# Kernel optimization log

Measured on AMD Instinct MI355X. Metric: run time of the kernel, lower is better.

The kernel has to match this reference:

```python
import jax, jax.numpy as jnp
import numpy as np

# ---------- static mesh topology helpers (numpy, setup-time only) ----------

def _topo_subdivide(nv, faces):
    edge_id = {}
    mids = []
    nf = []
    def mid(a, b):
        k = (a, b) if a < b else (b, a)
        if k not in edge_id:
            edge_id[k] = nv + len(mids)
            mids.append(k)
        return edge_id[k]
    for a, b, c in faces:
        a, b, c = int(a), int(b), int(c)
        ab, bc, ca = mid(a, b), mid(b, c), mid(c, a)
        nf += [[a, ab, ca], [b, bc, ab], [c, ca, bc], [ab, bc, ca]]
    return np.array(nf, dtype=np.int64), np.array(mids, dtype=np.int64)

def _icosphere(level, radius):
    t = (1.0 + 5.0 ** 0.5) / 2.0
    v = np.array([[-1, t, 0], [1, t, 0], [-1, -t, 0], [1, -t, 0],
                  [0, -1, t], [0, 1, t], [0, -1, -t], [0, 1, -t],
                  [t, 0, -1], [t, 0, 1], [-t, 0, -1], [-t, 0, 1]], dtype=np.float64)
    v /= np.linalg.norm(v, axis=1, keepdims=True)
    f = np.array([[0, 11, 5], [0, 5, 1], [0, 1, 7], [0, 7, 10], [0, 10, 11],
                  [1, 5, 9], [5, 11, 4], [11, 10, 2], [10, 7, 6], [7, 1, 8],
                  [3, 9, 4], [3, 4, 2], [3, 2, 6], [3, 6, 8], [3, 8, 9],
                  [4, 9, 5], [2, 4, 11], [6, 2, 10], [8, 6, 7], [9, 8, 1]], dtype=np.int64)
    for _ in range(level):
        f, mids = _topo_subdivide(len(v), f)
        mv = v[mids[:, 0]] + v[mids[:, 1]]
        mv /= np.linalg.norm(mv, axis=1, keepdims=True)
        v = np.concatenate([v, mv], 0)
    return (v * radius).astype(np.float32), f

def _directed_edges(faces):
    e = np.concatenate([faces[:, [0, 1]], faces[:, [1, 2]], faces[:, [2, 0]],
                        faces[:, [1, 0]], faces[:, [2, 1]], faces[:, [0, 2]]], 0)
    return np.unique(e, axis=0).T.astype(np.int64)  # (2, E) directed, deduped

# ---------- jax forward math ----------

def _project(verts, camera_c, camera_f):
    # K @ [I | t], t = (0,0,0.8): rows [f0,0,c0,0.8*c0],[0,f1,c1,0.8*c1],[0,0,1,0.8]
    z = jnp.zeros((), verts.dtype); o = jnp.ones((), verts.dtype)
    tz = jnp.asarray(0.8, verts.dtype)
    P = jnp.stack([
        jnp.stack([camera_f[0], z, camera_c[0], tz * camera_c[0]]),
        jnp.stack([z, camera_f[1], camera_c[1], tz * camera_c[1]]),
        jnp.stack([z, z, o, tz])])
    hom = jnp.concatenate([verts, jnp.ones((verts.shape[0], 1), verts.dtype)], 1)
    pc = hom @ P.T                     # (V, 3)
    return pc[:, :2] / pc[:, 2:3]      # (V, 2) pixel coords [x, y]

def _bilerp(feat, px, py, image_size):
    # feat: (C, dim, dim); px, py: (V,)
    dim = feat.shape[1]
    x = px * dim / image_size
    y = py * dim / image_size
    x1 = jnp.floor(x); x2 = x1 + 1.0
    y1 = jnp.floor(y); y2 = y1 + 1.0
    xi1 = jnp.clip(x1.astype(jnp.int32), 0, dim - 1)
    xi2 = jnp.clip(x2.astype(jnp.int32), 0, dim - 1)
    yi1 = jnp.clip(y1.astype(jnp.int32), 0, dim - 1)
    yi2 = jnp.clip(y2.astype(jnp.int32), 0, dim - 1)
    f11 = feat[:, xi1, yi1].T  # (V, C)
    f12 = feat[:, xi1, yi2].T
    f21 = feat[:, xi2, yi1].T
    f22 = feat[:, xi2, yi2].T
    w11 = ((x2 - x) * (y2 - y))[:, None]
    w12 = ((x2 - x) * (y - y1))[:, None]
    w21 = ((x - x1) * (y2 - y))[:, None]
    w22 = ((x - x1) * (y - y1))[:, None]
    return w11 * f11 + w12 * f12 + w21 * f21 + w22 * f22

def _gconv(x, W0, W1, b, src, dst):
    agg = jax.ops.segment_sum(x[dst], src, num_segments=x.shape[0])
    return x @ W0 + agg @ W1 + b

def _gresnet(x, edges, params):
    Win0, Win1, bin_, W0s, W1s, bs, Wc0, Wc1, bc = params
    src, dst = edges[0], edges[1]
    h = jax.nn.relu(_gconv(x, Win0, Win1, bin_, src, dst))
    def body(h, lw):
        W0, W1, b = lw
        return jax.nn.relu(_gconv(h, W0, W1, b, src, dst)) + h, None
    h, _ = jax.lax.scan(body, h, (W0s, W1s, bs))
    coords = _gconv(h, Wc0, Wc1, bc, src, dst)
    return h, coords

def _forward(f3, f4, f5, verts0, camera_c, camera_f, p1, p2, p3,
             edges1, edges2, edges3, mid0, mid1, image_size):
    def deform(verts, shape_feat, edges, params):
        pix = _project(verts, camera_c, camera_f)
        px, py = pix[:, 0], pix[:, 1]
        perc = jnp.concatenate([_bilerp(f3, px, py, image_size),
                                _bilerp(f4, px, py, image_size),
                                _bilerp(f5, px, py, image_size)], 1)  # (V, 1280)
        feats = jnp.concatenate([perc, shape_feat], 1)
        h, coords = _gresnet(feats, edges, params)
        return coords, h
    def unpool(verts, feat, mid):
        vf = jnp.concatenate([verts, feat], 1)
        new = (vf[mid[:, 0]] + vf[mid[:, 1]]) * 0.5  # edge midpoints
        vf = jnp.concatenate([vf, new], 0)
        return vf[:, :3], vf[:, 3:]
    verts, feat = deform(verts0, verts0, edges1, p1)
    verts, feat = unpool(verts, feat, mid0)
    verts, feat = deform(verts, feat, edges2, p2)
    verts, feat = unpool(verts, feat, mid1)
    verts, _ = deform(verts, feat, edges3, p3)
    return verts  # (40962, 3)

# ---------- harness entry points ----------

def setup_inputs() -> dict:
    key = jax.random.key(0)
    keys = iter(jax.random.split(key, 64))
    v0, f0 = _icosphere(4, 0.2)                      # 2562 verts, 5120 faces
    f1, mid0 = _topo_subdivide(len(v0), f0)          # -> 10242 verts topology
    f2, mid1 = _topo_subdivide(len(v0) + len(mid0), f1)  # -> 40962 verts
    inp = {
        'f3': jax.random.normal(next(keys), (256, 56, 56), jnp.float32),
        'f4': jax.random.normal(next(keys), (512, 28, 28), jnp.float32),
        'f5': jax.random.normal(next(keys), (512, 14, 14), jnp.float32),
        'verts0': jnp.asarray(v0),
        'camera_c': jnp.array([112.0, 112.0], jnp.float32),
        'camera_f': jnp.array([248.0, 248.0], jnp.float32),
    }
    D, L = 128, 12
    def stage(prefix, in_dim):
        def w(shape, scale):
            return jax.random.normal(next(keys), shape, jnp.float32) * scale
        inp[prefix + '_Win0'] = w((in_dim, D), 1.0 / np.sqrt(in_dim))
        inp[prefix + '_Win1'] = w((in_dim, D), 1.0 / np.sqrt(in_dim))
        inp[prefix + '_bin'] = jnp.zeros((D,), jnp.float32)
        inp[prefix + '_W0'] = w((L, D, D), 0.3 / np.sqrt(D))
        inp[prefix + '_W1'] = w((L, D, D), 0.3 / np.sqrt(D))
        inp[prefix + '_b'] = jnp.zeros((L, D), jnp.float32)
        inp[prefix + '_Wc0'] = w((D, 3), 0.01 / np.sqrt(D))
        inp[prefix + '_Wc1'] = w((D, 3), 0.01 / np.sqrt(D))
        inp[prefix + '_bc'] = jnp.zeros((3,), jnp.float32)
    stage('g1', 1283)
    stage('g2', 1408)
    stage('g3', 1408)
    inp['edges1'] = jnp.asarray(_directed_edges(f0))   # (2, 15360)
    inp['edges2'] = jnp.asarray(_directed_edges(f1))   # (2, 61440)
    inp['edges3'] = jnp.asarray(_directed_edges(f2))   # (2, 245760)
    inp['mid0'] = jnp.asarray(mid0)                    # (7680, 2)
    inp['mid1'] = jnp.asarray(mid1)                    # (30720, 2)
    inp['image_size'] = 224
    return inp

def reference(f3, f4, f5, verts0, camera_c, camera_f,
              g1_Win0, g1_Win1, g1_bin, g1_W0, g1_W1, g1_b, g1_Wc0, g1_Wc1, g1_bc,
              g2_Win0, g2_Win1, g2_bin, g2_W0, g2_W1, g2_b, g2_Wc0, g2_Wc1, g2_bc,
              g3_Win0, g3_Win1, g3_bin, g3_W0, g3_W1, g3_b, g3_Wc0, g3_Wc1, g3_bc,
              edges1, edges2, edges3, mid0, mid1, image_size):
    p1 = (g1_Win0, g1_Win1, g1_bin, g1_W0, g1_W1, g1_b, g1_Wc0, g1_Wc1, g1_bc)
    p2 = (g2_Win0, g2_Win1, g2_bin, g2_W0, g2_W1, g2_b, g2_Wc0, g2_Wc1, g2_bc)
    p3 = (g3_Win0, g3_Win1, g3_bin, g3_W0, g3_W1, g3_b, g3_Wc0, g3_Wc1, g3_bc)
    return _forward(f3, f4, f5, verts0, camera_c, camera_f, p1, p2, p3,
                    edges1, edges2, edges3, mid0, mid1, image_size)
```

## Files before the change

kernel.cpp:

```cpp
#include <hip/hip_runtime.h>
#include <hip/hip_bf16.h>
#include <cstddef>
#include <cstdint>

#define DIV_UP(a, b) (((a) + (b) - 1) / (b))

typedef __attribute__((ext_vector_type(8))) short bf16x8v;
typedef __attribute__((ext_vector_type(4))) float f32x4v;

__device__ __forceinline__ unsigned short bf16_rn(float v) {
    unsigned int u = __float_as_uint(v);
    unsigned int r = (u + 0x7FFFu + ((u >> 16) & 1u)) >> 16;
    return (unsigned short)r;
}
__device__ __forceinline__ float bf16_f(unsigned short h) {
    return __uint_as_float(((unsigned int)h) << 16);
}
__device__ __forceinline__ void f2hl(float v, unsigned short& hi, unsigned short& lo) {
    hi = bf16_rn(v);
    float r = v - bf16_f(hi);
    lo = bf16_rn(r);
}
__device__ __forceinline__ int xcd_swz(int orig, int nwg) {
    int q = nwg >> 3, r = nwg & 7;
    int xcd = orig & 7, idx = orig >> 3;
    return (xcd < r ? xcd * (q + 1) : r * (q + 1) + (xcd - r) * q) + idx;
}

__global__ void transpose_hl(const float* __restrict__ in, unsigned short* __restrict__ ohi,
                             unsigned short* __restrict__ olo, int C, int HW) {
    int idx = blockIdx.x * 256 + threadIdx.x;
    if (idx >= C * HW) return;
    int c = idx % C;
    int p = idx / C;
    float v = in[(size_t)c * HW + p];
    unsigned short hi, lo;
    f2hl(v, hi, lo);
    ohi[(size_t)p * C + c] = hi;
    olo[(size_t)p * C + c] = lo;
}

struct PackArgs {
    const float* Win0[3]; const float* Win1[3];
    const float* W0L[3];  const float* W1L[3];
    unsigned short *BtLhi[3], *BtLlo[3];
    unsigned short *BtShi[2], *BtSlo[2];
    unsigned short *Bgh[3], *Bgl[3];
};

__global__ void pack_all(PackArgs p) {
    const int LAY1 = 12 * 128 * 256;
    const int LAYT = 3 * LAY1;
    const int SH1 = 256 * 128;
    const int SHT = 2 * SH1;
    const int GB0 = 768 * 256, GB1 = 768 * 512;
    int idx = blockIdx.x * 256 + threadIdx.x;
    float v;
    unsigned short* dh;
    unsigned short* dl;
    size_t o;
    if (idx < LAYT) {
        int st = idx / LAY1, r = idx % LAY1;
        int l = r >> 15, rr = r & 32767;
        int n = rr >> 8, k = rr & 255;
        v = (k < 128) ? p.W0L[st][(size_t)l * 16384 + k * 128 + n]
                      : p.W1L[st][(size_t)l * 16384 + (k - 128) * 128 + n];
        dh = p.BtLhi[st]; dl = p.BtLlo[st]; o = r;
    } else if (idx < LAYT + SHT) {
        int q = idx - LAYT;
        int st = q / SH1, rr = q % SH1;
        int n = rr >> 7, k = rr & 127;
        const float* w0 = p.Win0[st + 1];
        const float* w1 = p.Win1[st + 1];
        v = (n < 128) ? w0[(size_t)(1280 + k) * 128 + n]
                      : w1[(size_t)(1280 + k) * 128 + (n - 128)];
        dh = p.BtShi[st]; dl = p.BtSlo[st]; o = rr;
    } else {
        int q = idx - LAYT - SHT;
        int m, C, base;
        if (q < GB0) { m = 0; C = 256; base = 0; }
        else if (q < GB0 + GB1) { m = 1; C = 512; base = 256; q -= GB0; }
        else if (q < GB0 + 2 * GB1) { m = 2; C = 512; base = 768; q -= GB0 + GB1; }
        else return;
        int n = q / C, k = q % C;
        int s = n >> 8, j = n & 255;
        v = (j < 128) ? p.Win0[s][(size_t)(base + k) * 128 + j]
                      : p.Win1[s][(size_t)(base + k) * 128 + (j - 128)];
        dh = p.Bgh[m]; dl = p.Bgl[m]; o = q;
    }
    unsigned short hi, lo;
    f2hl(v, hi, lo);
    dh[o] = hi;
    dl[o] = lo;
}

__global__ void desc_adj_kernel(const float* __restrict__ verts,
                                const float* __restrict__ cam_c, const float* __restrict__ cam_f,
                                const int* __restrict__ imgsz, int V,
                                const int* __restrict__ src, const int* __restrict__ dst, int E,
                                int* __restrict__ sampi, float* __restrict__ sampw,
                                int* __restrict__ adj8) {
    int v = blockIdx.x * 256 + threadIdx.x;
    if (v >= V) return;
    float X = verts[3 * v + 0], Yy = verts[3 * v + 1], Z = verts[3 * v + 2];
    float cx = cam_c[0], cy = cam_c[1], fx = cam_f[0], fy = cam_f[1];
    const float tz = 0.8f;
    float pz = Z + tz;
    float px = (fx * X + cx * Z + tz * cx) / pz;
    float py = (fy * Yy + cy * Z + tz * cy) / pz;
    float is = (float)imgsz[0];
    const int Ss[3] = {56, 28, 14};
#pragma unroll
    for (int m = 0; m < 3; ++m) {
        int S = Ss[m];
        float dim = (float)S;
        float x = px * dim / is;
        float y = py * dim / is;
        float x1 = floorf(x), y1 = floorf(y);
        float x2 = x1 + 1.0f, y2 = y1 + 1.0f;
        float smax = (float)(S - 1);
        int xi1 = (int)fminf(fmaxf(x1, 0.0f), smax);
        int xi2 = (int)fminf(fmaxf(x2, 0.0f), smax);
        int yi1 = (int)fminf(fmaxf(y1, 0.0f), smax);
        int yi2 = (int)fminf(fmaxf(y2, 0.0f), smax);
        int b = v * 12 + m * 4;
        sampi[b + 0] = xi1 * S + yi1;
        sampi[b + 1] = xi1 * S + yi2;
        sampi[b + 2] = xi2 * S + yi1;
        sampi[b + 3] = xi2 * S + yi2;
        sampw[b + 0] = (x2 - x) * (y2 - y);
        sampw[b + 1] = (x2 - x) * (y - y1);
        sampw[b + 2] = (x - x1) * (y2 - y);
        sampw[b + 3] = (x - x1) * (y - y1);
    }
    int lo = 0, hi = E;
    while (lo < hi) { int m = (lo + hi) >> 1; if (src[m] < v) lo = m + 1; else hi = m; }
    int e0 = lo;
    hi = E;
    while (lo < hi) { int m = (lo + hi) >> 1; if (src[m] < v + 1) lo = m + 1; else hi = m; }
    int e1 = lo;
    int* ap = adj8 + (size_t)v * 8;
#pragma unroll
    for (int i = 0; i < 8; ++i) {
        int e = e0 + i;
        ap[i] = (e < e1) ? dst[e] : -1;
    }
}

struct MArgs {
    const unsigned short *Ahi, *Alo; int lda;
    const unsigned short *Bhi, *Blo; int K;
    float* Y;
    int sstr;
    int V;
};

template <int EPI>
__global__ __launch_bounds__(256) void mgemm(MArgs g) {
    __shared__ unsigned short As_hi[64][40], As_lo[64][40];
    __shared__ unsigned short Bs_hi[128][40], Bs_lo[128][40];
    int tid = threadIdx.x;
    int row0 = blockIdx.y * 64;
    int col0 = blockIdx.x * 128;
    int l = tid & 63, wid = tid >> 6;
    int wr = wid & 1, wc = wid >> 1;
    int lw = l & 15, gg = l >> 4;
    f32x4v acc[2][4];
#pragma unroll
    for (int i = 0; i < 2; ++i)
#pragma unroll
        for (int j = 0; j < 4; ++j) acc[i][j] = (f32x4v){0.f, 0.f, 0.f, 0.f};

    int arow = tid >> 2, akoff = (tid & 3) * 8;
    for (int k0 = 0; k0 < g.K; k0 += 32) {
        __syncthreads();
        {
            int grow = row0 + arow;
            uint4 zh = make_uint4(0, 0, 0, 0), zl = make_uint4(0, 0, 0, 0);
            if (grow < g.V) {
                zh = *(const uint4*)(g.Ahi + (size_t)grow * g.lda + k0 + akoff);
                zl = *(const uint4*)(g.Alo + (size_t)grow * g.lda + k0 + akoff);
            }
            *(uint4*)&As_hi[arow][akoff] = zh;
            *(uint4*)&As_lo[arow][akoff] = zl;
        }
#pragma unroll
        for (int it = 0; it < 2; ++it) {
            int q = tid + it * 256;
            int n = q >> 2, koff = (q & 3) * 8;
            *(uint4*)&Bs_hi[n][koff] = *(const uint4*)(g.Bhi + (size_t)(col0 + n) * g.K + k0 + koff);
            *(uint4*)&Bs_lo[n][koff] = *(const uint4*)(g.Blo + (size_t)(col0 + n) * g.K + k0 + koff);
        }
        __syncthreads();
        bf16x8v ah[2], al[2], bh[4], bl[4];
#pragma unroll
        for (int mt = 0; mt < 2; ++mt) {
            int r = wr * 32 + mt * 16 + lw;
            ah[mt] = *(const bf16x8v*)&As_hi[r][gg * 8];
            al[mt] = *(const bf16x8v*)&As_lo[r][gg * 8];
        }
#pragma unroll
        for (int nt = 0; nt < 4; ++nt) {
            int c = wc * 64 + nt * 16 + lw;
            bh[nt] = *(const bf16x8v*)&Bs_hi[c][gg * 8];
            bl[nt] = *(const bf16x8v*)&Bs_lo[c][gg * 8];
        }
#pragma unroll
        for (int mt = 0; mt < 2; ++mt)
#pragma unroll
            for (int nt = 0; nt < 4; ++nt) {
                acc[mt][nt] = __builtin_amdgcn_mfma_f32_16x16x32_bf16(ah[mt], bh[nt], acc[mt][nt], 0, 0, 0);
                acc[mt][nt] = __builtin_amdgcn_mfma_f32_16x16x32_bf16(ah[mt], bl[nt], acc[mt][nt], 0, 0, 0);
                acc[mt][nt] = __builtin_amdgcn_mfma_f32_16x16x32_bf16(al[mt], bh[nt], acc[mt][nt], 0, 0, 0);
            }
    }
#pragma unroll
    for (int mt = 0; mt < 2; ++mt)
#pragma unroll
        for (int nt = 0; nt < 4; ++nt) {
            int colg = wc * 64 + nt * 16 + lw;
#pragma unroll
            for (int r = 0; r < 4; ++r) {
                int rowg = row0 + wr * 32 + mt * 16 + gg * 4 + r;
                if (rowg >= g.V) continue;
                float v = acc[mt][nt][r];
                if (EPI == 3) {
                    g.Y[(size_t)rowg * 256 + col0 + colg] = v;
                } else {
                    int cg = col0 + colg;
                    g.Y[(size_t)(cg >> 8) * g.sstr + (size_t)rowg * 256 + (cg & 255)] = v;
                }
            }
        }
}

__global__ void gather_kernel(const float* __restrict__ G, int sstr,
                              const int* __restrict__ sampi, const float* __restrict__ sampw,
                              float* __restrict__ Yb, int V, int stage,
                              const float* __restrict__ Win0, const float* __restrict__ Win1,
                              const float* __restrict__ shape) {
    int v = xcd_swz(blockIdx.x, gridDim.x);
    if (v >= V) return;
    int j = threadIdx.x;
    const float* Gs = G + (size_t)stage * sstr;
    int b = v * 12;
    float acc = (stage == 0) ? 0.0f : Yb[(size_t)v * 256 + j];
#pragma unroll
    for (int s = 0; s < 4; ++s)
        acc += sampw[b + s] * Gs[(size_t)sampi[b + s] * 256 + j];
#pragma unroll
    for (int s = 0; s < 4; ++s)
        acc += sampw[b + 4 + s] * Gs[(size_t)(3136 + sampi[b + 4 + s]) * 256 + j];
#pragma unroll
    for (int s = 0; s < 4; ++s)
        acc += sampw[b + 8 + s] * Gs[(size_t)(3920 + sampi[b + 8 + s]) * 256 + j];
    if (stage == 0) {
#pragma unroll
        for (int k = 0; k < 3; ++k) {
            float w = shape[v * 3 + k];
            float wv = (j < 128) ? Win0[(size_t)(1280 + k) * 128 + j]
                                 : Win1[(size_t)(1280 + k) * 128 + (j - 128)];
            acc += w * wv;
        }
    }
    Yb[(size_t)v * 256 + j] = acc;
}

__global__ __launch_bounds__(256) void combine_in(
    const float* __restrict__ Y, const float* __restrict__ bias,
    const int* __restrict__ adj8,
    float* __restrict__ hout, int V) {
    int bid = xcd_swz(blockIdx.x, gridDim.x);
    int v = bid * 2 + (threadIdx.x >> 7);
    int d = threadIdx.x & 127;
    if (v >= V) return;
    float val = Y[(size_t)v * 256 + d] + bias[d];
    const int* ap = adj8 + (size_t)v * 8;
    int n[6];
#pragma unroll
    for (int i = 0; i < 6; ++i) n[i] = ap[i];
#pragma unroll
    for (int i = 0; i < 6; ++i)
        if (n[i] >= 0) val += Y[(size_t)n[i] * 256 + 128 + d];
    val = fmaxf(val, 0.0f);
    hout[(size_t)v * 128 + d] = val;
}

struct LArgs {
    const float* h;
    const unsigned short *Bhi, *Blo;
    const int* adj8;
    const float* bias;
    float* hnext;
    int V;
};

__global__ __launch_bounds__(256) void lay_kernel(LArgs g) {
    __shared__ unsigned short As_hi[64][40], As_lo[64][40];
    __shared__ unsigned short Bs_hi[128][40], Bs_lo[128][40];
    int tid = threadIdx.x;
    int row0 = xcd_swz(blockIdx.x, gridDim.x) * 64;

    int l = tid & 63, wid = tid >> 6;
    int wr = wid & 1, wc = wid >> 1;
    int lw = l & 15, gg = l >> 4;
    int arow = tid >> 2;
    int aq = tid & 3;
    int grow = row0 + arow;

    f32x4v acc[2][4];
#pragma unroll
    for (int i = 0; i < 2; ++i)
#pragma unroll
        for (int j = 0; j < 4; ++j) acc[i][j] = (f32x4v){0.f, 0.f, 0.f, 0.f};

    float vals[32];

    auto mfma_step = [&](int ks, int kglob0) {
        uint4 b0h, b1h, b0l, b1l;
        {
            int n0 = tid >> 2, koff = (tid & 3) * 8;
            b0h = *(const uint4*)(g.Bhi + (size_t)n0 * 256 + kglob0 + koff);
            b0l = *(const uint4*)(g.Blo + (size_t)n0 * 256 + kglob0 + koff);
            int n1 = n0 + 64;
            b1h = *(const uint4*)(g.Bhi + (size_t)n1 * 256 + kglob0 + koff);
            b1l = *(const uint4*)(g.Blo + (size_t)n1 * 256 + kglob0 + koff);
        }
        if (aq == ks) {
            unsigned short hh[8], ll[8];
#pragma unroll
            for (int c = 0; c < 4; ++c) {
#pragma unroll
                for (int i = 0; i < 8; ++i) f2hl(vals[c * 8 + i], hh[i], ll[i]);
                *(uint4*)&As_hi[arow][c * 8] = *(uint4*)hh;
                *(uint4*)&As_lo[arow][c * 8] = *(uint4*)ll;
            }
        }
        {
            int n0 = tid >> 2, koff = (tid & 3) * 8;
            *(uint4*)&Bs_hi[n0][koff] = b0h;
            *(uint4*)&Bs_lo[n0][koff] = b0l;
            *(uint4*)&Bs_hi[n0 + 64][koff] = b1h;
            *(uint4*)&Bs_lo[n0 + 64][koff] = b1l;
        }
        __syncthreads();
        bf16x8v ah[2], al[2], bh[4], bl[4];
#pragma unroll
        for (int mt = 0; mt < 2; ++mt) {
            int r = wr * 32 + mt * 16 + lw;
            ah[mt] = *(const bf16x8v*)&As_hi[r][gg * 8];
            al[mt] = *(const bf16x8v*)&As_lo[r][gg * 8];
        }
#pragma unroll
        for (int nt = 0; nt < 4; ++nt) {
            int c = wc * 64 + nt * 16 + lw;
            bh[nt] = *(const bf16x8v*)&Bs_hi[c][gg * 8];
            bl[nt] = *(const bf16x8v*)&Bs_lo[c][gg * 8];
        }
#pragma unroll
        for (int mt = 0; mt < 2; ++mt)
#pragma unroll
            for (int nt = 0; nt < 4; ++nt) {
                acc[mt][nt] = __builtin_amdgcn_mfma_f32_16x16x32_bf16(ah[mt], bh[nt], acc[mt][nt], 0, 0, 0);
                acc[mt][nt] = __builtin_amdgcn_mfma_f32_16x16x32_bf16(ah[mt], bl[nt], acc[mt][nt], 0, 0, 0);
                acc[mt][nt] = __builtin_amdgcn_mfma_f32_16x16x32_bf16(al[mt], bh[nt], acc[mt][nt], 0, 0, 0);
            }
        __syncthreads();
    };

    if (grow < g.V) {
        const float* hp = g.h + (size_t)grow * 128 + aq * 32;
#pragma unroll
        for (int c = 0; c < 8; ++c) {
            float4 f = *(const float4*)(hp + c * 4);
            vals[c * 4 + 0] = f.x;
            vals[c * 4 + 1] = f.y;
            vals[c * 4 + 2] = f.z;
            vals[c * 4 + 3] = f.w;
        }
    } else {
#pragma unroll
        for (int i = 0; i < 32; ++i) vals[i] = 0.0f;
    }
    for (int ks = 0; ks < 4; ++ks) mfma_step(ks, ks * 32);

#pragma unroll
    for (int i = 0; i < 32; ++i) vals[i] = 0.0f;
    if (grow < g.V) {
        const int* ap = g.adj8 + (size_t)grow * 8;
        int n[6];
#pragma unroll
        for (int i = 0; i < 6; ++i) n[i] = ap[i];
#pragma unroll
        for (int i = 0; i < 6; ++i) {
            if (n[i] >= 0) {
                const float* hp = g.h + (size_t)n[i] * 128 + aq * 32;
#pragma unroll
                for (int c = 0; c < 8; ++c) {
                    float4 f = *(const float4*)(hp + c * 4);
                    vals[c * 4 + 0] += f.x;
                    vals[c * 4 + 1] += f.y;
                    vals[c * 4 + 2] += f.z;
                    vals[c * 4 + 3] += f.w;
                }
            }
        }
    }
    for (int ks = 0; ks < 4; ++ks) mfma_step(ks, 128 + ks * 32);

#pragma unroll
    for (int mt = 0; mt < 2; ++mt)
#pragma unroll
        for (int nt = 0; nt < 4; ++nt) {
            int colg = wc * 64 + nt * 16 + lw;
            float bv = g.bias[colg];
#pragma unroll
            for (int r = 0; r < 4; ++r) {
                int rowg = row0 + wr * 32 + mt * 16 + gg * 4 + r;
                if (rowg >= g.V) continue;
                float v = acc[mt][nt][r] + bv;
                v = fmaxf(v, 0.0f);
                v += g.h[(size_t)rowg * 128 + colg];
                g.hnext[(size_t)rowg * 128 + colg] = v;
            }
        }
}

__global__ void coordgemm_kernel(const float* __restrict__ h,
                                 const float* __restrict__ Wc0, const float* __restrict__ Wc1,
                                 int V, float* __restrict__ Yc) {
    int idx = blockIdx.x * 256 + threadIdx.x;
    if (idx >= V * 6) return;
    int v = idx / 6, j = idx % 6;
    const float* W = (j < 3) ? Wc0 : Wc1;
    int jj = (j < 3) ? j : j - 3;
    const float* hp = h + (size_t)v * 128;
    float acc = 0.0f;
#pragma unroll
    for (int k = 0; k < 32; ++k) {
        float4 f = *(const float4*)(hp + k * 4);
        acc += f.x * W[(k * 4 + 0) * 3 + jj];
        acc += f.y * W[(k * 4 + 1) * 3 + jj];
        acc += f.z * W[(k * 4 + 2) * 3 + jj];
        acc += f.w * W[(k * 4 + 3) * 3 + jj];
    }
    Yc[idx] = acc;
}

__global__ void coordcombine_kernel(const float* __restrict__ Yc, const float* __restrict__ bc,
                                    const int* __restrict__ adj8,
                                    int V, float* __restrict__ out) {
    int idx = blockIdx.x * 256 + threadIdx.x;
    if (idx >= V * 3) return;
    int v = idx / 3, j = idx % 3;
    float val = Yc[(size_t)v * 6 + j] + bc[j];
    const int* ap = adj8 + (size_t)v * 8;
    int n[6];
#pragma unroll
    for (int i = 0; i < 6; ++i) n[i] = ap[i];
#pragma unroll
    for (int i = 0; i < 6; ++i)
        if (n[i] >= 0) val += Yc[(size_t)n[i] * 6 + 3 + j];
    out[(size_t)v * 3 + j] = val;
}

__global__ void unpool_kernel(float* __restrict__ verts, const float* __restrict__ h,
                              const int* __restrict__ mid, int V, int Nm,
                              unsigned short* __restrict__ fphi, unsigned short* __restrict__ fplo) {
    int r = blockIdx.x;
    int t = threadIdx.x;
    if (r < V) {
        float v = h[(size_t)r * 128 + t];
        unsigned short hi, lo;
        f2hl(v, hi, lo);
        fphi[(size_t)r * 128 + t] = hi;
        fplo[(size_t)r * 128 + t] = lo;
    } else {
        int i = r - V;
        int a = mid[2 * i], b = mid[2 * i + 1];
        float v = 0.5f * (h[(size_t)a * 128 + t] + h[(size_t)b * 128 + t]);
        unsigned short hi, lo;
        f2hl(v, hi, lo);
        fphi[(size_t)r * 128 + t] = hi;
        fplo[(size_t)r * 128 + t] = lo;
        if (t < 3)
            verts[(size_t)r * 3 + t] = 0.5f * (verts[(size_t)a * 3 + t] + verts[(size_t)b * 3 + t]);
    }
}

extern "C" void kernel_launch(void* const* d_in, const int* in_sizes, int n_in,
                              void* d_out, int out_size, void* d_ws, size_t ws_size,
                              hipStream_t stream) {
    const float* f3 = (const float*)d_in[0];
    const float* f4 = (const float*)d_in[1];
    const float* f5 = (const float*)d_in[2];
    const float* verts0 = (const float*)d_in[3];
    const float* cam_c = (const float*)d_in[4];
    const float* cam_f = (const float*)d_in[5];
    const int* imgsz = (const int*)d_in[38];

    int V0 = in_sizes[3] / 3;
    int E[3] = {in_sizes[33] / 2, in_sizes[34] / 2, in_sizes[35] / 2};
    int Nm0 = in_sizes[36] / 2, Nm1 = in_sizes[37] / 2;
    int V1 = V0 + Nm0, V2 = V1 + Nm1;
    int Vs[3] = {V0, V1, V2};
    const int NPIXT = 3136 + 784 + 196;
    const int GS = NPIXT * 256;

    char* wsp = (char*)d_ws;
    auto alloc = [&](size_t bytes) -> void* {
        void* p = (void*)wsp;
        wsp += (bytes + 255) & ~(size_t)255;
        return p;
    };
    unsigned short* ft0h = (unsigned short*)alloc((size_t)3136 * 256 * 2);
    unsigned short* ft0l = (unsigned short*)alloc((size_t)3136 * 256 * 2);
    unsigned short* ft1h = (unsigned short*)alloc((size_t)784 * 512 * 2);
    unsigned short* ft1l = (unsigned short*)alloc((size_t)784 * 512 * 2);
    unsigned short* ft2h = (unsigned short*)alloc((size_t)196 * 512 * 2);
    unsigned short* ft2l = (unsigned short*)alloc((size_t)196 * 512 * 2);
    unsigned short* Bg0h = (unsigned short*)alloc((size_t)768 * 256 * 2);
    unsigned short* Bg0l = (unsigned short*)alloc((size_t)768 * 256 * 2);
    unsigned short* Bg1h = (unsigned short*)alloc((size_t)768 * 512 * 2);
    unsigned short* Bg1l = (unsigned short*)alloc((size_t)768 * 512 * 2);
    unsigned short* Bg2h = (unsigned short*)alloc((size_t)768 * 512 * 2);
    unsigned short* Bg2l = (unsigned short*)alloc((size_t)768 * 512 * 2);
    float* Gbuf = (float*)alloc((size_t)3 * GS * 4);
    unsigned short* BtLhi[3];
    unsigned short* BtLlo[3];
    for (int s = 0; s < 3; ++s) {
        BtLhi[s] = (unsigned short*)alloc((size_t)12 * 128 * 256 * 2);
        BtLlo[s] = (unsigned short*)alloc((size_t)12 * 128 * 256 * 2);
    }
    unsigned short* BtShi[2];
    unsigned short* BtSlo[2];
    for (int s = 0; s < 2; ++s) {
        BtShi[s] = (unsigned short*)alloc((size_t)256 * 128 * 2);
        BtSlo[s] = (unsigned short*)alloc((size_t)256 * 128 * 2);
    }
    float* Ybuf = (float*)alloc((size_t)V2 * 256 * 4);
    float* hA = (float*)alloc((size_t)V2 * 128 * 4);
    float* hB = (float*)alloc((size_t)V2 * 128 * 4);
    unsigned short* FPhi = (unsigned short*)alloc((size_t)V2 * 128 * 2);
    unsigned short* FPlo = (unsigned short*)alloc((size_t)V2 * 128 * 2);
    float* vertsbuf = (float*)alloc((size_t)V2 * 3 * 4);
    float* Yc = (float*)alloc((size_t)V2 * 6 * 4);
    int* sampi = (int*)alloc((size_t)V2 * 12 * 4);
    float* sampw = (float*)alloc((size_t)V2 * 12 * 4);
    int* adj8 = (int*)alloc((size_t)V2 * 8 * 4);

    transpose_hl<<<DIV_UP(256 * 56 * 56, 256), 256, 0, stream>>>(f3, ft0h, ft0l, 256, 56 * 56);
    transpose_hl<<<DIV_UP(512 * 28 * 28, 256), 256, 0, stream>>>(f4, ft1h, ft1l, 512, 28 * 28);
    transpose_hl<<<DIV_UP(512 * 14 * 14, 256), 256, 0, stream>>>(f5, ft2h, ft2l, 512, 14 * 14);

    {
        PackArgs p;
        for (int s = 0; s < 3; ++s) {
            p.Win0[s] = (const float*)d_in[6 + s * 9 + 0];
            p.Win1[s] = (const float*)d_in[6 + s * 9 + 1];
            p.W0L[s] = (const float*)d_in[6 + s * 9 + 3];
            p.W1L[s] = (const float*)d_in[6 + s * 9 + 4];
            p.BtLhi[s] = BtLhi[s]; p.BtLlo[s] = BtLlo[s];
        }
        p.BtShi[0] = BtShi[0]; p.BtSlo[0] = BtSlo[0];
        p.BtShi[1] = BtShi[1]; p.BtSlo[1] = BtSlo[1];
        p.Bgh[0] = Bg0h; p.Bgl[0] = Bg0l;
        p.Bgh[1] = Bg1h; p.Bgl[1] = Bg1l;
        p.Bgh[2] = Bg2h; p.Bgl[2] = Bg2l;
        int total = 3 * 12 * 128 * 256 + 2 * 256 * 128 + 768 * 256 + 2 * 768 * 512;
        pack_all<<<DIV_UP(total, 256), 256, 0, stream>>>(p);
    }

    {
        MArgs m = {};
        m.sstr = GS;
        m.Ahi = ft0h; m.Alo = ft0l; m.lda = 256;
        m.Bhi = Bg0h; m.Blo = Bg0l; m.K = 256;
        m.Y = Gbuf; m.V = 3136;
        dim3 g0(6, DIV_UP(3136, 64));
        mgemm<2><<<g0, 256, 0, stream>>>(m);
        m.Ahi = ft1h; m.Alo = ft1l; m.lda = 512;
        m.Bhi = Bg1h; m.Blo = Bg1l; m.K = 512;
        m.Y = Gbuf + (size_t)3136 * 256; m.V = 784;
        dim3 g1(6, DIV_UP(784, 64));
        mgemm<2><<<g1, 256, 0, stream>>>(m);
        m.Ahi = ft2h; m.Alo = ft2l; m.lda = 512;
        m.Bhi = Bg2h; m.Blo = Bg2l; m.K = 512;
        m.Y = Gbuf + (size_t)3920 * 256; m.V = 196;
        dim3 g2(6, DIV_UP(196, 64));
        mgemm<2><<<g2, 256, 0, stream>>>(m);
    }

    for (int si = 0; si < 3; ++si) {
        const float* Win0 = (const float*)d_in[6 + si * 9 + 0];
        const float* Win1 = (const float*)d_in[6 + si * 9 + 1];
        const float* bin = (const float*)d_in[6 + si * 9 + 2];
        const float* bs = (const float*)d_in[6 + si * 9 + 5];
        const float* Wc0 = (const float*)d_in[6 + si * 9 + 6];
        const float* Wc1 = (const float*)d_in[6 + si * 9 + 7];
        const float* bc = (const float*)d_in[6 + si * 9 + 8];
        const int* edges = (const int*)d_in[33 + si];
        int Ecur = E[si];
        const int* esrc = edges;
        const int* edst = edges + Ecur;
        int V = Vs[si];
        const float* vertsin = (si == 0) ? verts0 : vertsbuf;

        desc_adj_kernel<<<DIV_UP(V, 256), 256, 0, stream>>>(vertsin, cam_c, cam_f, imgsz, V,
                                                            esrc, edst, Ecur, sampi, sampw, adj8);
        if (si > 0) {
            MArgs m = {};
            m.Ahi = FPhi; m.Alo = FPlo; m.lda = 128;
            m.Bhi = BtShi[si - 1]; m.Blo = BtSlo[si - 1]; m.K = 128;
            m.Y = Ybuf; m.V = V;
            dim3 grid(2, DIV_UP(V, 64));
            mgemm<3><<<grid, 256, 0, stream>>>(m);
        }
        gather_kernel<<<V, 256, 0, stream>>>(Gbuf, GS, sampi, sampw, Ybuf, V, si, Win0, Win1,
                                             (si == 0) ? verts0 : nullptr);
        combine_in<<<DIV_UP(V, 2), 256, 0, stream>>>(Ybuf, bin, adj8, hA, V);

        float* hcur = hA;
        float* hnext = hB;
        for (int ll = 0; ll < 12; ++ll) {
            LArgs a = {};
            a.h = hcur;
            a.Bhi = BtLhi[si] + (size_t)ll * 32768;
            a.Blo = BtLlo[si] + (size_t)ll * 32768;
            a.adj8 = adj8;
            a.bias = bs + (size_t)ll * 128;
            a.hnext = hnext;
            a.V = V;
            lay_kernel<<<DIV_UP(V, 64), 256, 0, stream>>>(a);
            float* t = hcur; hcur = hnext; hnext = t;
        }

        coordgemm_kernel<<<DIV_UP(V * 6, 256), 256, 0, stream>>>(hcur, Wc0, Wc1, V, Yc);
        float* ctarget = (si == 2) ? (float*)d_out : vertsbuf;
        coordcombine_kernel<<<DIV_UP(V * 3, 256), 256, 0, stream>>>(Yc, bc, adj8, V, ctarget);
        if (si < 2) {
            const int* mid = (const int*)d_in[36 + si];
            int Nm = (si == 0) ? Nm0 : Nm1;
            unpool_kernel<<<V + Nm, 128, 0, stream>>>(vertsbuf, hcur, mid, V, Nm, FPhi, FPlo);
        }
    }
}
```

Measured before the change: 1.418 ms.

## Restructure graph-conv layer kernel to per-wave 16-row tiles without LDS

```diff
diff --git a/kernel.cpp b/kernel.cpp
--- a/kernel.cpp
+++ b/kernel.cpp
@@ -239,51 +239,69 @@
                               float* __restrict__ Yb, int V, int stage,
                               const float* __restrict__ Win0, const float* __restrict__ Win1,
                               const float* __restrict__ shape) {
-    int v = xcd_swz(blockIdx.x, gridDim.x);
+    int v = xcd_swz(blockIdx.x, gridDim.x) * 4 + (threadIdx.x >> 6);
     if (v >= V) return;
-    int j = threadIdx.x;
+    int j = (threadIdx.x & 63) * 4;
     const float* Gs = G + (size_t)stage * sstr;
     int b = v * 12;
-    float acc = (stage == 0) ? 0.0f : Yb[(size_t)v * 256 + j];
-#pragma unroll
-    for (int s = 0; s < 4; ++s)
-        acc += sampw[b + s] * Gs[(size_t)sampi[b + s] * 256 + j];
-#pragma unroll
-    for (int s = 0; s < 4; ++s)
-        acc += sampw[b + 4 + s] * Gs[(size_t)(3136 + sampi[b + 4 + s]) * 256 + j];
-#pragma unroll
-    for (int s = 0; s < 4; ++s)
-        acc += sampw[b + 8 + s] * Gs[(size_t)(3920 + sampi[b + 8 + s]) * 256 + j];
+    float4 acc;
+    if (stage == 0) acc = make_float4(0.f, 0.f, 0.f, 0.f);
+    else acc = *(const float4*)(Yb + (size_t)v * 256 + j);
+#pragma unroll
+    for (int s = 0; s < 4; ++s) {
+        float w = sampw[b + s];
+        float4 f = *(const float4*)(Gs + (size_t)sampi[b + s] * 256 + j);
+        acc.x += w * f.x; acc.y += w * f.y; acc.z += w * f.z; acc.w += w * f.w;
+    }
+#pragma unroll
+    for (int s = 0; s < 4; ++s) {
+        float w = sampw[b + 4 + s];
+        float4 f = *(const float4*)(Gs + (size_t)(3136 + sampi[b + 4 + s]) * 256 + j);
+        acc.x += w * f.x; acc.y += w * f.y; acc.z += w * f.z; acc.w += w * f.w;
+    }
+#pragma unroll
+    for (int s = 0; s < 4; ++s) {
+        float w = sampw[b + 8 + s];
+        float4 f = *(const float4*)(Gs + (size_t)(3920 + sampi[b + 8 + s]) * 256 + j);
+        acc.x += w * f.x; acc.y += w * f.y; acc.z += w * f.z; acc.w += w * f.w;
+    }
     if (stage == 0) {
 #pragma unroll
         for (int k = 0; k < 3; ++k) {
             float w = shape[v * 3 + k];
-            float wv = (j < 128) ? Win0[(size_t)(1280 + k) * 128 + j]
-                                 : Win1[(size_t)(1280 + k) * 128 + (j - 128)];
-            acc += w * wv;
-        }
-    }
-    Yb[(size_t)v * 256 + j] = acc;
+            const float* wr = (j < 128) ? Win0 + (size_t)(1280 + k) * 128 + j
+                                        : Win1 + (size_t)(1280 + k) * 128 + (j - 128);
+            float4 wv = *(const float4*)wr;
+            acc.x += w * wv.x; acc.y += w * wv.y; acc.z += w * wv.z; acc.w += w * wv.w;
+        }
+    }
+    *(float4*)(Yb + (size_t)v * 256 + j) = acc;
 }
 
 __global__ __launch_bounds__(256) void combine_in(
     const float* __restrict__ Y, const float* __restrict__ bias,
     const int* __restrict__ adj8,
     float* __restrict__ hout, int V) {
-    int bid = xcd_swz(blockIdx.x, gridDim.x);
-    int v = bid * 2 + (threadIdx.x >> 7);
-    int d = threadIdx.x & 127;
+    int v = xcd_swz(blockIdx.x, gridDim.x) * 8 + (threadIdx.x >> 5);
     if (v >= V) return;
-    float val = Y[(size_t)v * 256 + d] + bias[d];
+    int d = (threadIdx.x & 31) * 4;
+    float4 val = *(const float4*)(Y + (size_t)v * 256 + d);
+    float4 b4 = *(const float4*)(bias + d);
+    val.x += b4.x; val.y += b4.y; val.z += b4.z; val.w += b4.w;
     const int* ap = adj8 + (size_t)v * 8;
     int n[6];
 #pragma unroll
     for (int i = 0; i < 6; ++i) n[i] = ap[i];
 #pragma unroll
-    for (int i = 0; i < 6; ++i)
-        if (n[i] >= 0) val += Y[(size_t)n[i] * 256 + 128 + d];
-    val = fmaxf(val, 0.0f);
-    hout[(size_t)v * 128 + d] = val;
+    for (int i = 0; i < 6; ++i) {
+        if (n[i] >= 0) {
+            float4 f = *(const float4*)(Y + (size_t)n[i] * 256 + 128 + d);
+            val.x += f.x; val.y += f.y; val.z += f.z; val.w += f.w;
+        }
+    }
+    val.x = fmaxf(val.x, 0.f); val.y = fmaxf(val.y, 0.f);
+    val.z = fmaxf(val.z, 0.f); val.w = fmaxf(val.w, 0.f);
+    *(float4*)(hout + (size_t)v * 128 + d) = val;
 }
 
 struct LArgs {
@@ -296,134 +314,97 @@
 };
 
 __global__ __launch_bounds__(256) void lay_kernel(LArgs g) {
-    __shared__ unsigned short As_hi[64][40], As_lo[64][40];
-    __shared__ unsigned short Bs_hi[128][40], Bs_lo[128][40];
     int tid = threadIdx.x;
-    int row0 = xcd_swz(blockIdx.x, gridDim.x) * 64;
-
-    int l = tid & 63, wid = tid >> 6;
-    int wr = wid & 1, wc = wid >> 1;
-    int lw = l & 15, gg = l >> 4;
-    int arow = tid >> 2;
-    int aq = tid & 3;
-    int grow = row0 + arow;
-
-    f32x4v acc[2][4];
-#pragma unroll
-    for (int i = 0; i < 2; ++i)
-#pragma unroll
-        for (int j = 0; j < 4; ++j) acc[i][j] = (f32x4v){0.f, 0.f, 0.f, 0.f};
-
-    float vals[32];
-
-    auto mfma_step = [&](int ks, int kglob0) {
-        uint4 b0h, b1h, b0l, b1l;
-        {
-            int n0 = tid >> 2, koff = (tid & 3) * 8;
-            b0h = *(const uint4*)(g.Bhi + (size_t)n0 * 256 + kglob0 + koff);
-            b0l = *(const uint4*)(g.Blo + (size_t)n0 * 256 + kglob0 + koff);
-            int n1 = n0 + 64;
-            b1h = *(const uint4*)(g.Bhi + (size_t)n1 * 256 + kglob0 + koff);
-            b1l = *(const uint4*)(g.Blo + (size_t)n1 * 256 + kglob0 + koff);
-        }
-        if (aq == ks) {
-            unsigned short hh[8], ll[8];
-#pragma unroll
-            for (int c = 0; c < 4; ++c) {
-#pragma unroll
-                for (int i = 0; i < 8; ++i) f2hl(vals[c * 8 + i], hh[i], ll[i]);
-                *(uint4*)&As_hi[arow][c * 8] = *(uint4*)hh;
-                *(uint4*)&As_lo[arow][c * 8] = *(uint4*)ll;
-            }
-        }
-        {
-            int n0 = tid >> 2, koff = (tid & 3) * 8;
-            *(uint4*)&Bs_hi[n0][koff] = b0h;
-            *(uint4*)&Bs_lo[n0][koff] = b0l;
-            *(uint4*)&Bs_hi[n0 + 64][koff] = b1h;
-            *(uint4*)&Bs_lo[n0 + 64][koff] = b1l;
-        }
-        __syncthreads();
-        bf16x8v ah[2], al[2], bh[4], bl[4];
-#pragma unroll
-        for (int mt = 0; mt < 2; ++mt) {
-            int r = wr * 32 + mt * 16 + lw;
-            ah[mt] = *(const bf16x8v*)&As_hi[r][gg * 8];
-            al[mt] = *(const bf16x8v*)&As_lo[r][gg * 8];
-        }
-#pragma unroll
-        for (int nt = 0; nt < 4; ++nt) {
-            int c = wc * 64 + nt * 16 + lw;
-            bh[nt] = *(const bf16x8v*)&Bs_hi[c][gg * 8];
-            bl[nt] = *(const bf16x8v*)&Bs_lo[c][gg * 8];
-        }
-#pragma unroll
-        for (int mt = 0; mt < 2; ++mt)
-#pragma unroll
-            for (int nt = 0; nt < 4; ++nt) {
-                acc[mt][nt] = __builtin_amdgcn_mfma_f32_16x16x32_bf16(ah[mt], bh[nt], acc[mt][nt], 0, 0, 0);
-                acc[mt][nt] = __builtin_amdgcn_mfma_f32_16x16x32_bf16(ah[mt], bl[nt], acc[mt][nt], 0, 0, 0);
-                acc[mt][nt] = __builtin_amdgcn_mfma_f32_16x16x32_bf16(al[mt], bh[nt], acc[mt][nt], 0, 0, 0);
-            }
-        __syncthreads();
+    int wid = tid >> 6, l = tid & 63;
+    int rowbase = (xcd_swz(blockIdx.x, gridDim.x) * 4 + wid) * 16;
+    int lrow = l & 15, lks = l >> 4;
+    int grow = rowbase + lrow;
+    bool act = grow < g.V;
+
+    f32x4v acc[8];
+#pragma unroll
+    for (int nt = 0; nt < 8; ++nt) acc[nt] = (f32x4v){0.f, 0.f, 0.f, 0.f};
+
+    const float* hrow = g.h + (size_t)grow * 128;
+    int n[6];
+    if (act) {
+        const int* ap = g.adj8 + (size_t)grow * 8;
+#pragma unroll
+        for (int i = 0; i < 6; ++i) n[i] = ap[i];
+    } else {
+#pragma unroll
+        for (int i = 0; i < 6; ++i) n[i] = -1;
+    }
+
+    const unsigned short* Bh = g.Bhi + lrow * 256;
+    const unsigned short* Bl = g.Blo + lrow * 256;
+
+    auto do_step = [&](int kb, const float* a) {
+        unsigned short hh[8], ll[8];
+#pragma unroll
+        for (int i = 0; i < 8; ++i) f2hl(a[i], hh[i], ll[i]);
+        bf16x8v ah = *(const bf16x8v*)hh;
+        bf16x8v al = *(const bf16x8v*)ll;
+#pragma unroll
+        for (int nt = 0; nt < 8; ++nt) {
+            bf16x8v bh = *(const bf16x8v*)(Bh + nt * 4096 + kb);
+            bf16x8v bl = *(const bf16x8v*)(Bl + nt * 4096 + kb);
+            acc[nt] = __builtin_amdgcn_mfma_f32_16x16x32_bf16(ah, bh, acc[nt], 0, 0, 0);
+            acc[nt] = __builtin_amdgcn_mfma_f32_16x16x32_bf16(ah, bl, acc[nt], 0, 0, 0);
+            acc[nt] = __builtin_amdgcn_mfma_f32_16x16x32_bf16(al, bh, acc[nt], 0, 0, 0);
+        }
     };
 
-    if (grow < g.V) {
-        const float* hp = g.h + (size_t)grow * 128 + aq * 32;
-#pragma unroll
-        for (int c = 0; c < 8; ++c) {
-            float4 f = *(const float4*)(hp + c * 4);
-            vals[c * 4 + 0] = f.x;
-            vals[c * 4 + 1] = f.y;
-            vals[c * 4 + 2] = f.z;
-            vals[c * 4 + 3] = f.w;
-        }
-    } else {
-#pragma unroll
-        for (int i = 0; i < 32; ++i) vals[i] = 0.0f;
-    }
-    for (int ks = 0; ks < 4; ++ks) mfma_step(ks, ks * 32);
-
-#pragma unroll
-    for (int i = 0; i < 32; ++i) vals[i] = 0.0f;
-    if (grow < g.V) {
-        const int* ap = g.adj8 + (size_t)grow * 8;
-        int n[6];
-#pragma unroll
-        for (int i = 0; i < 6; ++i) n[i] = ap[i];
+#pragma unroll
+    for (int ks = 0; ks < 4; ++ks) {
+        int kb = ks * 32 + lks * 8;
+        float a[8];
+        if (act) {
+            float4 f0 = *(const float4*)(hrow + kb);
+            float4 f1 = *(const float4*)(hrow + kb + 4);
+            a[0] = f0.x; a[1] = f0.y; a[2] = f0.z; a[3] = f0.w;
+            a[4] = f1.x; a[5] = f1.y; a[6] = f1.z; a[7] = f1.w;
+        } else {
+#pragma unroll
+            for (int i = 0; i < 8; ++i) a[i] = 0.f;
+        }
+        do_step(kb, a);
+    }
+
+#pragma unroll
+    for (int ks = 0; ks < 4; ++ks) {
+        int ko = ks * 32 + lks * 8;
+        float a[8];
+#pragma unroll
+        for (int i = 0; i < 8; ++i) a[i] = 0.f;
 #pragma unroll
         for (int i = 0; i < 6; ++i) {
             if (n[i] >= 0) {
-                const float* hp = g.h + (size_t)n[i] * 128 + aq * 32;
-#pragma unroll
-                for (int c = 0; c < 8; ++c) {
-                    float4 f = *(const float4*)(hp + c * 4);
-                    vals[c * 4 + 0] += f.x;
-                    vals[c * 4 + 1] += f.y;
-                    vals[c * 4 + 2] += f.z;
-                    vals[c * 4 + 3] += f.w;
-                }
+                const float* hp = g.h + (size_t)n[i] * 128 + ko;
+                float4 f0 = *(const float4*)hp;
+                float4 f1 = *(const float4*)(hp + 4);
+                a[0] += f0.x; a[1] += f0.y; a[2] += f0.z; a[3] += f0.w;
+                a[4] += f1.x; a[5] += f1.y; a[6] += f1.z; a[7] += f1.w;
             }
         }
-    }
-    for (int ks = 0; ks < 4; ++ks) mfma_step(ks, 128 + ks * 32);
-
-#pragma unroll
-    for (int mt = 0; mt < 2; ++mt)
-#pragma unroll
-        for (int nt = 0; nt < 4; ++nt) {
-            int colg = wc * 64 + nt * 16 + lw;
-            float bv = g.bias[colg];
-#pragma unroll
-            for (int r = 0; r < 4; ++r) {
-                int rowg = row0 + wr * 32 + mt * 16 + gg * 4 + r;
-                if (rowg >= g.V) continue;
-                float v = acc[mt][nt][r] + bv;
+        do_step(128 + ko, a);
+    }
+
+#pragma unroll
+    for (int nt = 0; nt < 8; ++nt) {
+        int colg = nt * 16 + lrow;
+        float bv = g.bias[colg];
+#pragma unroll
+        for (int r = 0; r < 4; ++r) {
+            int rowg = rowbase + lks * 4 + r;
+            if (rowg < g.V) {
+                float v = acc[nt][r] + bv;
                 v = fmaxf(v, 0.0f);
                 v += g.h[(size_t)rowg * 128 + colg];
                 g.hnext[(size_t)rowg * 128 + colg] = v;
             }
         }
+    }
 }
 
 __global__ void coordgemm_kernel(const float* __restrict__ h,
@@ -616,9 +597,9 @@
             dim3 grid(2, DIV_UP(V, 64));
             mgemm<3><<<grid, 256, 0, stream>>>(m);
         }
-        gather_kernel<<<V, 256, 0, stream>>>(Gbuf, GS, sampi, sampw, Ybuf, V, si, Win0, Win1,
-                                             (si == 0) ? verts0 : nullptr);
-        combine_in<<<DIV_UP(V, 2), 256, 0, stream>>>(Ybuf, bin, adj8, hA, V);
+        gather_kernel<<<DIV_UP(V, 4), 256, 0, stream>>>(Gbuf, GS, sampi, sampw, Ybuf, V, si,
+                                                        Win0, Win1, (si == 0) ? verts0 : nullptr);
+        combine_in<<<DIV_UP(V, 8), 256, 0, stream>>>(Ybuf, bin, adj8, hA, V);
 
         float* hcur = hA;
         float* hnext = hB;
```

Measured after the change: 2.131 ms. 50.3% more time.
